# Kernel optimization log

Measured on AMD Instinct MI355X. Metric: run time of the kernel, lower is better.

The kernel has to match this reference:

```python
import jax, jax.numpy as jnp
import numpy as np

DIM = 256
FOCAL_LEVELS = (3, 5, 7)  # odd kernels so padding=k//2 preserves length
B, L = 8, 16384


def _dwconv(x, k):
    # x: [B, C, L], k: [C, 1, K] depthwise kernel (groups=C)
    pad = k.shape[-1] // 2
    return jax.lax.conv_general_dilated(
        x, k, window_strides=(1,), padding=[(pad, pad)],
        dimension_numbers=('NCH', 'OIH', 'NCH'),
        feature_group_count=x.shape[1])


def setup_inputs() -> dict:
    key = jax.random.key(0)
    ks = jax.random.split(key, 13)
    C = DIM
    G = len(FOCAL_LEVELS) + 1
    s = jnp.float32(0.02)
    inp = {
        'x': jax.random.normal(ks[0], (B, C, L), jnp.float32),
        'q_w': jax.random.normal(ks[1], (C, C), jnp.float32) * s,
        'q_b': jax.random.normal(ks[2], (C,), jnp.float32) * s,
        'v_w': jax.random.normal(ks[3], (C, C), jnp.float32) * s,
        'v_b': jax.random.normal(ks[4], (C,), jnp.float32) * s,
        'g_w': jax.random.normal(ks[5], (G, C), jnp.float32) * s,
        'g_b': jax.random.normal(ks[6], (G,), jnp.float32) * s,
        'f0_w': jax.random.normal(ks[7], (C, 1, FOCAL_LEVELS[0]), jnp.float32) * s,
        'f1_w': jax.random.normal(ks[8], (C, 1, FOCAL_LEVELS[1]), jnp.float32) * s,
        'f2_w': jax.random.normal(ks[9], (C, 1, FOCAL_LEVELS[2]), jnp.float32) * s,
        'mix_w': jax.random.normal(ks[10], (C, C), jnp.float32) * s,
        'mix_b': jax.random.normal(ks[11], (C,), jnp.float32) * s,
    }
    return inp


def reference(x, q_w, q_b, v_w, v_b, g_w, g_b, f0_w, f1_w, f2_w, mix_w, mix_b):
    gelu = lambda t: jax.nn.gelu(t, approximate=False)  # torch GELU default = exact erf
    # Linear weights are [out, in]; contract over channel axis of [B, C, L]
    focus = jnp.einsum('bcl,ec->bel', x, v_w) + v_b[None, :, None]   # [B, C, L]
    gates = jnp.einsum('bcl,gc->bgl', x, g_w) + g_b[None, :, None]   # [B, 4, L]
    query = jnp.einsum('bcl,ec->bel', x, q_w) + q_b[None, :, None]   # [B, C, L]

    kernels = (f0_w, f1_w, f2_w)  # fixed small set: loop over levels is fine
    focus = gelu(_dwconv(focus, kernels[0]))
    acc = focus * gates[:, 0:1, :]
    for i in range(1, len(kernels)):
        focus = gelu(_dwconv(focus, kernels[i]))
        acc = acc + focus * gates[:, i:i + 1, :]

    # global focus: mean over length, GELU, broadcast across length via gate
    global_focus = gelu(jnp.mean(focus, axis=2, keepdims=True))      # [B, C, 1]
    acc = acc + global_focus * gates[:, len(kernels):len(kernels) + 1, :]

    # mix_depth: 1x1 conv == pointwise linear over channels
    acc = jnp.einsum('bcl,oc->bol', acc, mix_w) + mix_b[None, :, None]
    mask = jax.nn.softmax(acc, axis=-1)  # softmax over length
    out = jax.nn.sigmoid(query) * mask
    return (out, mask)
```

## Files before the change

kernel.cpp:

```cpp
#include <hip/hip_runtime.h>

#define LLEN 16384
#define PAD 258

typedef short bf16x8 __attribute__((ext_vector_type(8)));
typedef float f32x4 __attribute__((ext_vector_type(4)));

__device__ __forceinline__ unsigned bfbits(float f) {
  union { float f; unsigned u; } v; v.f = f;
  return (v.u + 0x7FFFu + ((v.u >> 16) & 1u)) >> 16;
}
__device__ __forceinline__ short f2bf(float f) { return (short)bfbits(f); }
__device__ __forceinline__ float bf2f(short s) {
  union { unsigned u; float f; } v;
  v.u = ((unsigned)(unsigned short)s) << 16;
  return v.f;
}
__device__ __forceinline__ float geluf(float x) {
  return 0.5f * x * (1.0f + erff(x * 0.70710678118654752f));
}
__device__ __forceinline__ float gelu_fast(float x) {
  return x / (1.0f + __expf(-1.702f * x));
}
__device__ __forceinline__ float waveRedSum(float v) {
  #pragma unroll
  for (int o = 32; o > 0; o >>= 1) v += __shfl_xor(v, o, 64);
  return v;
}

__global__ __launch_bounds__(256) void k0_convert(
    const float* __restrict__ qw, const float* __restrict__ vw,
    const float* __restrict__ gw, const float* __restrict__ mw,
    short* __restrict__ qwb, short* __restrict__ vwb,
    short* __restrict__ gwb, short* __restrict__ mwb,
    float* __restrict__ rowsum) {
  int idx = blockIdx.x * 256 + threadIdx.x;
  qwb[idx] = f2bf(qw[idx]);
  vwb[idx] = f2bf(vw[idx]);
  mwb[idx] = f2bf(mw[idx]);
  if (idx < 4096) {
    int r = idx >> 8, c = idx & 255;
    gwb[idx] = (r < 4) ? f2bf(gw[r * 256 + c]) : (short)0;
  }
  if (idx < 2048) rowsum[idx] = 0.f;
}

__device__ __forceinline__ void gemm64(const short* __restrict__ wmat,
                                       const short xs[64][PAD], int lane,
                                       f32x4 acc[4][4]) {
  int r = lane & 15, h = lane >> 4;
  #pragma unroll
  for (int k0 = 0; k0 < 256; k0 += 32) {
    bf16x8 xfr[4];
    #pragma unroll
    for (int lf = 0; lf < 4; ++lf)
      xfr[lf] = *(const bf16x8*)&xs[lf * 16 + r][k0 + 8 * h];
    #pragma unroll
    for (int ef = 0; ef < 4; ++ef) {
      bf16x8 wfr = *(const bf16x8*)(wmat + (ef * 16 + r) * 256 + k0 + 8 * h);
      #pragma unroll
      for (int lf = 0; lf < 4; ++lf)
        acc[ef][lf] = __builtin_amdgcn_mfma_f32_16x16x32_bf16(xfr[lf], wfr,
                                                              acc[ef][lf], 0, 0, 0);
    }
  }
}

__device__ __forceinline__ void store_bf4(short* p, f32x4 a, float bias) {
  uint2 pk;
  pk.x = bfbits(a[0] + bias) | (bfbits(a[1] + bias) << 16);
  pk.y = bfbits(a[2] + bias) | (bfbits(a[3] + bias) << 16);
  *(uint2*)p = pk;
}

__global__ __launch_bounds__(256) void k1_qvg(
    const float* __restrict__ x, const short* __restrict__ vwb,
    const short* __restrict__ qwb, const short* __restrict__ gwb,
    const float* __restrict__ v_b, const float* __restrict__ q_b,
    const float* __restrict__ g_b, short* __restrict__ focus0,
    short* __restrict__ qzS, float* __restrict__ gates) {
  int b = blockIdx.x >> 8, lt = blockIdx.x & 255;
  int l0 = lt << 6;
  __shared__ short xs[64][PAD];
  int t = threadIdx.x;
  {
    int l2 = (t & 31) * 2, cg = t >> 5;
    const float* xb = x + ((size_t)b << 22) + l0 + l2;
    #pragma unroll 4
    for (int rep = 0; rep < 16; ++rep) {
      int c = rep * 16 + cg * 2;
      float2 a = *(const float2*)&xb[(size_t)c << 14];
      float2 bb = *(const float2*)&xb[((size_t)c + 1) << 14];
      *(unsigned*)&xs[l2][c] = bfbits(a.x) | (bfbits(bb.x) << 16);
      *(unsigned*)&xs[l2 + 1][c] = bfbits(a.y) | (bfbits(bb.y) << 16);
    }
  }
  __syncthreads();
  int lane = t & 63, wave = t >> 6;
  int r = lane & 15, h = lane >> 4;
  int e0 = wave << 6;
  f32x4 acc[4][4];

  #pragma unroll
  for (int ef = 0; ef < 4; ++ef)
    #pragma unroll
    for (int lf = 0; lf < 4; ++lf)
      acc[ef][lf] = (f32x4){0.f, 0.f, 0.f, 0.f};
  gemm64(vwb + e0 * 256, xs, lane, acc);
  #pragma unroll
  for (int ef = 0; ef < 4; ++ef) {
    int e = e0 + ef * 16 + r;
    float bias = v_b[e];
    short* rowp = focus0 + ((size_t)((b << 8) | e) << 14) + l0 + 4 * h;
    #pragma unroll
    for (int lf = 0; lf < 4; ++lf)
      store_bf4(rowp + lf * 16, acc[ef][lf], bias);
  }

  #pragma unroll
  for (int ef = 0; ef < 4; ++ef)
    #pragma unroll
    for (int lf = 0; lf < 4; ++lf)
      acc[ef][lf] = (f32x4){0.f, 0.f, 0.f, 0.f};
  gemm64(qwb + e0 * 256, xs, lane, acc);
  #pragma unroll
  for (int ef = 0; ef < 4; ++ef) {
    int e = e0 + ef * 16 + r;
    float bias = q_b[e];
    short* rowp = qzS + (((size_t)((b << 8) | e) << 15) + 16384) + l0 + 4 * h;
    #pragma unroll
    for (int lf = 0; lf < 4; ++lf)
      store_bf4(rowp + lf * 16, acc[ef][lf], bias);
  }

  if (wave == 0) {
    f32x4 gacc[4];
    #pragma unroll
    for (int lf = 0; lf < 4; ++lf) gacc[lf] = (f32x4){0.f, 0.f, 0.f, 0.f};
    #pragma unroll
    for (int k0 = 0; k0 < 256; k0 += 32) {
      bf16x8 wfr = *(const bf16x8*)(gwb + r * 256 + k0 + 8 * h);
      #pragma unroll
      for (int lf = 0; lf < 4; ++lf) {
        bf16x8 xfr = *(const bf16x8*)&xs[lf * 16 + r][k0 + 8 * h];
        gacc[lf] = __builtin_amdgcn_mfma_f32_16x16x32_bf16(xfr, wfr, gacc[lf], 0, 0, 0);
      }
    }
    if (r < 4) {
      float gb = g_b[r];
      float* gp = gates + (((size_t)((b << 2) | r)) << 14) + l0 + 4 * h;
      #pragma unroll
      for (int lf = 0; lf < 4; ++lf) {
        float4 o = {gacc[lf][0] + gb, gacc[lf][1] + gb,
                    gacc[lf][2] + gb, gacc[lf][3] + gb};
        *(float4*)(gp + lf * 16) = o;
      }
    }
  }
}

__global__ __launch_bounds__(256) void k2_conv(
    const short* __restrict__ focus0, const float* __restrict__ gates,
    const float* __restrict__ f0_w, const float* __restrict__ f1_w,
    const float* __restrict__ f2_w, short* __restrict__ acc3S,
    float* __restrict__ rowsum) {
  int bx = blockIdx.x;
  int b = bx >> 12, c = (bx >> 4) & 255, lt = bx & 15;
  int l0 = lt << 10;
  __shared__ float s0[1036], s1[1034], s2[1030];
  __shared__ float rs[4];
  int t = threadIdx.x;
  const short* fp = focus0 + ((size_t)((b << 8) | c) << 14);
  if (lt > 0 && lt < 15) {
    const unsigned* fp2 = (const unsigned*)(fp + l0 - 6);
    for (int i2 = t; i2 < 518; i2 += 256) {
      unsigned u = fp2[i2];
      s0[2 * i2] = bf2f((short)(u & 0xFFFF));
      s0[2 * i2 + 1] = bf2f((short)(u >> 16));
    }
  } else {
    for (int i = t; i < 1036; i += 256) {
      int gl = l0 - 6 + i;
      s0[i] = (gl >= 0 && gl < LLEN) ? bf2f(fp[gl]) : 0.f;
    }
  }
  float w0[3], w1[5], w2[7];
  #pragma unroll
  for (int j = 0; j < 3; ++j) w0[j] = f0_w[c * 3 + j];
  #pragma unroll
  for (int j = 0; j < 5; ++j) w1[j] = f1_w[c * 5 + j];
  #pragma unroll
  for (int j = 0; j < 7; ++j) w2[j] = f2_w[c * 7 + j];
  __syncthreads();
  for (int i = t; i < 1034; i += 256) {
    int gl = l0 - 5 + i;
    float z = w0[0] * s0[i] + w0[1] * s0[i + 1] + w0[2] * s0[i + 2];
    s1[i] = (gl >= 0 && gl < LLEN) ? gelu_fast(z) : 0.f;
  }
  __syncthreads();
  for (int i = t; i < 1030; i += 256) {
    int gl = l0 - 3 + i;
    float z = w1[0] * s1[i] + w1[1] * s1[i + 1] + w1[2] * s1[i + 2] +
              w1[3] * s1[i + 3] + w1[4] * s1[i + 4];
    s2[i] = (gl >= 0 && gl < LLEN) ? gelu_fast(z) : 0.f;
  }
  __syncthreads();
  const float* gp = gates + ((size_t)(b << 2) << 14);
  short* op = acc3S + ((size_t)((b << 8) | c) << 15);
  float lsum = 0.f;
  #pragma unroll
  for (int ii = 0; ii < 2; ++ii) {
    int i = 2 * t + 512 * ii;
    float z0 = w2[0] * s2[i] + w2[1] * s2[i + 1] + w2[2] * s2[i + 2] +
               w2[3] * s2[i + 3] + w2[4] * s2[i + 4] + w2[5] * s2[i + 5] +
               w2[6] * s2[i + 6];
    float z1 = w2[0] * s2[i + 1] + w2[1] * s2[i + 2] + w2[2] * s2[i + 3] +
               w2[3] * s2[i + 4] + w2[4] * s2[i + 5] + w2[5] * s2[i + 6] +
               w2[6] * s2[i + 7];
    float f30 = gelu_fast(z0), f31 = gelu_fast(z1);
    lsum += f30 + f31;
    int l = l0 + i;
    float a0 = s1[i + 5] * gp[l] + s2[i + 3] * gp[LLEN + l] + f30 * gp[2 * LLEN + l];
    float a1 = s1[i + 6] * gp[l + 1] + s2[i + 4] * gp[LLEN + l + 1] +
               f31 * gp[2 * LLEN + l + 1];
    *(unsigned*)&op[l] = bfbits(a0) | (bfbits(a1) << 16);
  }
  float wsv = waveRedSum(lsum);
  if ((t & 63) == 0) rs[t >> 6] = wsv;
  __syncthreads();
  if (t == 0) atomicAdd(&rowsum[(b << 8) | c], rs[0] + rs[1] + rs[2] + rs[3]);
}

__global__ __launch_bounds__(256) void k4_mix(
    short* maskS, const float* __restrict__ gates, const float* __restrict__ rowsum,
    const short* __restrict__ mwb, const float* __restrict__ mix_b) {
  int b = blockIdx.x >> 8, lt = blockIdx.x & 255;
  int l0 = lt << 6;
  __shared__ short xs[64][PAD];
  __shared__ float gfS[256];
  int t = threadIdx.x;
  gfS[t] = geluf(rowsum[(b << 8) | t] * (1.0f / 16384.0f));
  __syncthreads();
  {
    int l2 = (t & 31) * 2, cg = t >> 5;
    float2 g3v = *(const float2*)(gates + (((size_t)((b << 2) | 3)) << 14) + l0 + l2);
    const unsigned short* ap =
        (const unsigned short*)maskS + (((size_t)(b << 8)) << 15) + l0 + l2;
    #pragma unroll 4
    for (int rep = 0; rep < 16; ++rep) {
      int c = rep * 16 + cg * 2;
      unsigned av = *(const unsigned*)&ap[(size_t)c << 15];
      unsigned bv = *(const unsigned*)&ap[((size_t)c + 1) << 15];
      float gfa = gfS[c], gfb = gfS[c + 1];
      float a0 = bf2f((short)(av & 0xFFFF)) + gfa * g3v.x;
      float a1 = bf2f((short)(av >> 16)) + gfa * g3v.y;
      float b0 = bf2f((short)(bv & 0xFFFF)) + gfb * g3v.x;
      float b1 = bf2f((short)(bv >> 16)) + gfb * g3v.y;
      *(unsigned*)&xs[l2][c] = bfbits(a0) | (bfbits(b0) << 16);
      *(unsigned*)&xs[l2 + 1][c] = bfbits(a1) | (bfbits(b1) << 16);
    }
  }
  __syncthreads();
  int lane = t & 63, wave = t >> 6;
  int r = lane & 15, h = lane >> 4;
  int e0 = wave << 6;
  f32x4 acc[4][4];
  #pragma unroll
  for (int ef = 0; ef < 4; ++ef)
    #pragma unroll
    for (int lf = 0; lf < 4; ++lf)
      acc[ef][lf] = (f32x4){0.f, 0.f, 0.f, 0.f};
  gemm64(mwb + e0 * 256, xs, lane, acc);
  #pragma unroll
  for (int ef = 0; ef < 4; ++ef) {
    int o = e0 + ef * 16 + r;
    float bias = mix_b[o];
    short* rowp = maskS + (((size_t)((b << 8) | o) << 15) + 16384) + l0 + 4 * h;
    #pragma unroll
    for (int lf = 0; lf < 4; ++lf)
      store_bf4(rowp + lf * 16, acc[ef][lf], bias);
  }
}

__global__ __launch_bounds__(512) void k5_softmax(
    const short* __restrict__ maskS, const short* __restrict__ outS,
    float* __restrict__ maskF, float* __restrict__ outF) {
  int row = blockIdx.x;
  int t = threadIdx.x;
  const short* mrow = maskS + ((size_t)row << 15) + 16384;
  const short* qrow = outS + ((size_t)row << 15) + 16384;
  float* mw = maskF + ((size_t)row << 14);
  float* ow = outF + ((size_t)row << 14);
  int lane = t & 63, wave = t >> 6;
  bf16x8 qv[4];
  float f[32];
  float lm = -3.0e38f;
  #pragma unroll
  for (int i = 0; i < 4; ++i) {
    bf16x8 mv = *(const bf16x8*)&mrow[i * 4096 + t * 8];
    qv[i] = *(const bf16x8*)&qrow[i * 4096 + t * 8];
    #pragma unroll
    for (int j = 0; j < 8; ++j) {
      float vf = bf2f(mv[j]);
      f[i * 8 + j] = vf;
      lm = fmaxf(lm, vf);
    }
  }
  __shared__ float redm[8], reds[8];
  {
    #pragma unroll
    for (int o = 32; o > 0; o >>= 1) lm = fmaxf(lm, __shfl_xor(lm, o, 64));
  }
  if (lane == 0) redm[wave] = lm;
  __syncthreads();
  float M = redm[0];
  #pragma unroll
  for (int w = 1; w < 8; ++w) M = fmaxf(M, redm[w]);
  float ls = 0.f;
  #pragma unroll
  for (int k = 0; k < 32; ++k) {
    f[k] = __expf(f[k] - M);
    ls += f[k];
  }
  float wsum = waveRedSum(ls);
  if (lane == 0) reds[wave] = wsum;
  __syncthreads();
  float S = reds[0];
  #pragma unroll
  for (int w = 1; w < 8; ++w) S += reds[w];
  float inv = 1.0f / S;
  #pragma unroll
  for (int i = 0; i < 4; ++i) {
    float mk[8], oo[8];
    #pragma unroll
    for (int j = 0; j < 8; ++j) {
      mk[j] = f[i * 8 + j] * inv;
      float sig = 1.0f / (1.0f + __expf(-bf2f(qv[i][j])));
      oo[j] = sig * mk[j];
    }
    float* mp = &mw[i * 4096 + t * 8];
    float* op = &ow[i * 4096 + t * 8];
    *(float4*)mp = (float4){mk[0], mk[1], mk[2], mk[3]};
    *(float4*)(mp + 4) = (float4){mk[4], mk[5], mk[6], mk[7]};
    *(float4*)op = (float4){oo[0], oo[1], oo[2], oo[3]};
    *(float4*)(op + 4) = (float4){oo[4], oo[5], oo[6], oo[7]};
  }
}

extern "C" void kernel_launch(void* const* d_in, const int* in_sizes, int n_in,
                              void* d_out, int out_size, void* d_ws, size_t ws_size,
                              hipStream_t stream) {
  const float* x     = (const float*)d_in[0];
  const float* q_w   = (const float*)d_in[1];
  const float* q_b   = (const float*)d_in[2];
  const float* v_w   = (const float*)d_in[3];
  const float* v_b   = (const float*)d_in[4];
  const float* g_w   = (const float*)d_in[5];
  const float* g_b   = (const float*)d_in[6];
  const float* f0_w  = (const float*)d_in[7];
  const float* f1_w  = (const float*)d_in[8];
  const float* f2_w  = (const float*)d_in[9];
  const float* mix_w = (const float*)d_in[10];
  const float* mix_b = (const float*)d_in[11];

  float* outbuf  = (float*)d_out;
  float* maskbuf = outbuf + (size_t)8 * 256 * 16384;
  short* outS  = (short*)outbuf;
  short* maskS = (short*)maskbuf;

  char* ws = (char*)d_ws;
  short* vwb    = (short*)(ws + 0);
  short* qwb    = (short*)(ws + 131072);
  short* mwb    = (short*)(ws + 262144);
  short* gwb    = (short*)(ws + 393216);
  float* rowsum = (float*)(ws + 401408);
  float* gates  = (float*)(ws + 417792);
  short* focus0 = (short*)(ws + 2514944);

  k0_convert<<<dim3(256), dim3(256), 0, stream>>>(q_w, v_w, g_w, mix_w,
                                                  qwb, vwb, gwb, mwb, rowsum);
  k1_qvg<<<dim3(2048), dim3(256), 0, stream>>>(x, vwb, qwb, gwb, v_b, q_b, g_b,
                                               focus0, outS, gates);
  k2_conv<<<dim3(32768), dim3(256), 0, stream>>>(focus0, gates, f0_w, f1_w, f2_w,
                                                 maskS, rowsum);
  k4_mix<<<dim3(2048), dim3(256), 0, stream>>>(maskS, gates, rowsum, mwb, mix_b);
  k5_softmax<<<dim3(2048), dim3(512), 0, stream>>>(maskS, outS, maskbuf, outbuf);
}
```

Measured before the change: 365.8 us.

## Pretranspose x into bf16 tiles and fold global-focus term into mix epilogue

Adds a separate transpose kernel that converts x to bf16 in a tile-contiguous layout stored in the mask output buffer, so k1 can load its shared-memory tile with contiguous vector reads. The global-focus contribution is moved algebraically past the mix GEMM. A tiny kernel computes mix_w·gelu(mean) per batch, and k4 adds wg*gate3 in its epilogue instead of adding it to every input element before the GEMM. This removes strided fp32 loads and per-element work from the GEMM prologues, at the cost of an extra kernel launch and an extra write-plus-read pass over x in bf16. The epilogue also uses the fp32 mix weights for the global term, which changes rounding slightly.

Measured after the change: 417.4 us. 14.1% more time.

```diff
diff --git a/kernel.cpp b/kernel.cpp
--- a/kernel.cpp
+++ b/kernel.cpp
@@ -45,6 +45,34 @@
   if (idx < 2048) rowsum[idx] = 0.f;
 }
 
+__global__ __launch_bounds__(256) void k0t_transpose(
+    const float* __restrict__ x, short* __restrict__ maskS) {
+  int tile = blockIdx.x;
+  int b = tile >> 8, lt = tile & 255;
+  int l0 = lt << 6;
+  __shared__ short ts[64][PAD];
+  int t = threadIdx.x;
+  const float* xb = x + ((size_t)b << 22) + l0;
+  int cg = t >> 4;
+  int le = (t & 15) * 4;
+  #pragma unroll 4
+  for (int k = 0; k < 16; ++k) {
+    int c = k * 16 + cg;
+    float4 v = *(const float4*)&xb[((size_t)c << 14) + le];
+    ts[le + 0][c] = f2bf(v.x);
+    ts[le + 1][c] = f2bf(v.y);
+    ts[le + 2][c] = f2bf(v.z);
+    ts[le + 3][c] = f2bf(v.w);
+  }
+  __syncthreads();
+  short* out = maskS + ((size_t)tile << 15) + 16384;
+  #pragma unroll
+  for (int i = 0; i < 8; ++i) {
+    int p = i * 2048 + t * 8;
+    *(bf16x8*)&out[p] = *(const bf16x8*)&ts[p >> 8][p & 255];
+  }
+}
+
 __device__ __forceinline__ void gemm64(const short* __restrict__ wmat,
                                        const short xs[64][PAD], int lane,
                                        f32x4 acc[4][4]) {
@@ -74,7 +102,7 @@
 }
 
 __global__ __launch_bounds__(256) void k1_qvg(
-    const float* __restrict__ x, const short* __restrict__ vwb,
+    const short* __restrict__ xtS, const short* __restrict__ vwb,
     const short* __restrict__ qwb, const short* __restrict__ gwb,
     const float* __restrict__ v_b, const float* __restrict__ q_b,
     const float* __restrict__ g_b, short* __restrict__ focus0,
@@ -84,15 +112,11 @@
   __shared__ short xs[64][PAD];
   int t = threadIdx.x;
   {
-    int l2 = (t & 31) * 2, cg = t >> 5;
-    const float* xb = x + ((size_t)b << 22) + l0 + l2;
-    #pragma unroll 4
-    for (int rep = 0; rep < 16; ++rep) {
-      int c = rep * 16 + cg * 2;
-      float2 a = *(const float2*)&xb[(size_t)c << 14];
-      float2 bb = *(const float2*)&xb[((size_t)c + 1) << 14];
-      *(unsigned*)&xs[l2][c] = bfbits(a.x) | (bfbits(bb.x) << 16);
-      *(unsigned*)&xs[l2 + 1][c] = bfbits(a.y) | (bfbits(bb.y) << 16);
+    const short* xt = xtS + ((size_t)blockIdx.x << 15) + 16384;
+    #pragma unroll
+    for (int i = 0; i < 8; ++i) {
+      int p = i * 2048 + t * 8;
+      *(bf16x8*)&xs[p >> 8][p & 255] = *(const bf16x8*)&xt[p];
     }
   }
   __syncthreads();
@@ -231,33 +255,37 @@
   if (t == 0) atomicAdd(&rowsum[(b << 8) | c], rs[0] + rs[1] + rs[2] + rs[3]);
 }
 
+__global__ __launch_bounds__(256) void k3b_wgf(
+    const float* __restrict__ rowsum, const float* __restrict__ mix_w,
+    float* __restrict__ wgf) {
+  int b = blockIdx.x;
+  int t = threadIdx.x;
+  __shared__ float gf_s[256];
+  gf_s[t] = geluf(rowsum[(b << 8) | t] * (1.0f / 16384.0f));
+  __syncthreads();
+  const float* wrow = mix_w + t * 256;
+  float s = 0.f;
+  #pragma unroll 8
+  for (int c = 0; c < 256; ++c) s += wrow[c] * gf_s[c];
+  wgf[(b << 8) | t] = s;
+}
+
 __global__ __launch_bounds__(256) void k4_mix(
-    short* maskS, const float* __restrict__ gates, const float* __restrict__ rowsum,
+    short* maskS, const float* __restrict__ gates, const float* __restrict__ wgf,
     const short* __restrict__ mwb, const float* __restrict__ mix_b) {
   int b = blockIdx.x >> 8, lt = blockIdx.x & 255;
   int l0 = lt << 6;
   __shared__ short xs[64][PAD];
-  __shared__ float gfS[256];
-  int t = threadIdx.x;
-  gfS[t] = geluf(rowsum[(b << 8) | t] * (1.0f / 16384.0f));
-  __syncthreads();
+  int t = threadIdx.x;
   {
-    int l2 = (t & 31) * 2, cg = t >> 5;
-    float2 g3v = *(const float2*)(gates + (((size_t)((b << 2) | 3)) << 14) + l0 + l2);
-    const unsigned short* ap =
-        (const unsigned short*)maskS + (((size_t)(b << 8)) << 15) + l0 + l2;
-    #pragma unroll 4
-    for (int rep = 0; rep < 16; ++rep) {
-      int c = rep * 16 + cg * 2;
-      unsigned av = *(const unsigned*)&ap[(size_t)c << 15];
-      unsigned bv = *(const unsigned*)&ap[((size_t)c + 1) << 15];
-      float gfa = gfS[c], gfb = gfS[c + 1];
-      float a0 = bf2f((short)(av & 0xFFFF)) + gfa * g3v.x;
-      float a1 = bf2f((short)(av >> 16)) + gfa * g3v.y;
-      float b0 = bf2f((short)(bv & 0xFFFF)) + gfb * g3v.x;
-      float b1 = bf2f((short)(bv >> 16)) + gfb * g3v.y;
-      *(unsigned*)&xs[l2][c] = bfbits(a0) | (bfbits(b0) << 16);
-      *(unsigned*)&xs[l2 + 1][c] = bfbits(a1) | (bfbits(b1) << 16);
+    int c = t;
+    const unsigned short* arow =
+        (const unsigned short*)maskS + (((size_t)((b << 8) | c)) << 15) + l0;
+    #pragma unroll
+    for (int i = 0; i < 8; ++i) {
+      bf16x8 v = *(const bf16x8*)&arow[i * 8];
+      #pragma unroll
+      for (int j = 0; j < 8; ++j) xs[i * 8 + j][c] = v[j];
     }
   }
   __syncthreads();
@@ -271,14 +299,26 @@
     for (int lf = 0; lf < 4; ++lf)
       acc[ef][lf] = (f32x4){0.f, 0.f, 0.f, 0.f};
   gemm64(mwb + e0 * 256, xs, lane, acc);
+  float4 g3v[4];
+  #pragma unroll
+  for (int lf = 0; lf < 4; ++lf)
+    g3v[lf] = *(const float4*)&gates[(((size_t)((b << 2) | 3)) << 14) + l0 +
+                                     lf * 16 + 4 * h];
   #pragma unroll
   for (int ef = 0; ef < 4; ++ef) {
     int o = e0 + ef * 16 + r;
-    float bias = mix_b[o];
+    float base = mix_b[o];
+    float wg = wgf[(b << 8) | o];
     short* rowp = maskS + (((size_t)((b << 8) | o) << 15) + 16384) + l0 + 4 * h;
     #pragma unroll
-    for (int lf = 0; lf < 4; ++lf)
-      store_bf4(rowp + lf * 16, acc[ef][lf], bias);
+    for (int lf = 0; lf < 4; ++lf) {
+      uint2 pk;
+      pk.x = bfbits(acc[ef][lf][0] + base + wg * g3v[lf].x) |
+             (bfbits(acc[ef][lf][1] + base + wg * g3v[lf].y) << 16);
+      pk.y = bfbits(acc[ef][lf][2] + base + wg * g3v[lf].z) |
+             (bfbits(acc[ef][lf][3] + base + wg * g3v[lf].w) << 16);
+      *(uint2*)(rowp + lf * 16) = pk;
+    }
   }
 }
 
@@ -374,15 +414,18 @@
   short* mwb    = (short*)(ws + 262144);
   short* gwb    = (short*)(ws + 393216);
   float* rowsum = (float*)(ws + 401408);
+  float* wgf    = (float*)(ws + 409600);
   float* gates  = (float*)(ws + 417792);
   short* focus0 = (short*)(ws + 2514944);
 
   k0_convert<<<dim3(256), dim3(256), 0, stream>>>(q_w, v_w, g_w, mix_w,
                                                   qwb, vwb, gwb, mwb, rowsum);
-  k1_qvg<<<dim3(2048), dim3(256), 0, stream>>>(x, vwb, qwb, gwb, v_b, q_b, g_b,
-                                               focus0, outS, gates);
+  k0t_transpose<<<dim3(2048), dim3(256), 0, stream>>>(x, maskS);
+  k1_qvg<<<dim3(2048), dim3(256), 0, stream>>>(maskS, vwb, qwb, gwb, v_b, q_b,
+                                               g_b, focus0, outS, gates);
   k2_conv<<<dim3(32768), dim3(256), 0, stream>>>(focus0, gates, f0_w, f1_w, f2_w,
                                                  maskS, rowsum);
-  k4_mix<<<dim3(2048), dim3(256), 0, stream>>>(maskS, gates, rowsum, mwb, mix_b);
+  k3b_wgf<<<dim3(8), dim3(256), 0, stream>>>(rowsum, mix_w, wgf);
+  k4_mix<<<dim3(2048), dim3(256), 0, stream>>>(maskS, gates, wgf, mwb, mix_b);
   k5_softmax<<<dim3(2048), dim3(512), 0, stream>>>(maskS, outS, maskbuf, outbuf);
 }
```
